# Kernel tuning notes

Measured on AMD Instinct MI355X. Metric: run time of the kernel, lower is better.

## Reference

```python
import jax, jax.numpy as jnp
import numpy as np

B, T, F, H = 256, 512, 8, 256
DEC_STEPS = 35
BN_EPS = 1e-3


def setup_inputs() -> dict:
    key = jax.random.key(0)
    ks = jax.random.split(key, 16)
    s = 0.05
    return {
        "pulse": jax.random.normal(ks[0], (B, T, F), jnp.float32),
        "bn_gamma": jax.random.uniform(ks[1], (F,), jnp.float32, 0.5, 1.5),
        "bn_beta": jax.random.normal(ks[2], (F,), jnp.float32) * s,
        "bn_mean": jax.random.normal(ks[3], (F,), jnp.float32) * s,
        "bn_var": jax.random.uniform(ks[4], (F,), jnp.float32, 0.5, 1.5),
        "W_pe": jax.random.normal(ks[5], (F, H), jnp.float32) * s,
        "b_pe": jax.random.normal(ks[6], (H,), jnp.float32) * s,
        "embed_table": jax.random.normal(ks[7], (1, H), jnp.float32) * s,
        "W_x": jax.random.normal(ks[8], (H, 4 * H), jnp.float32) * s,
        "W_h": jax.random.normal(ks[9], (H, 4 * H), jnp.float32) * s,
        "b_lstm": jax.random.normal(ks[10], (4 * H,), jnp.float32) * s,
        "W_mlp": jax.random.normal(ks[11], (H, 2), jnp.float32) * s,
        "b_mlp": jax.random.normal(ks[12], (2,), jnp.float32) * s,
        "scale_w": jax.random.normal(ks[13], (1, 1, 2), jnp.float32),
        "scale_b": jax.random.normal(ks[14], (1, 1, 2), jnp.float32),
    }


def _lstm_cell(x, h, c, W_x, W_h, b):
    # Keras LSTMCell: gate order i, f, g(cell), o
    z = x @ W_x + h @ W_h + b  # (B, 4H)
    i, f, g, o = jnp.split(z, 4, axis=-1)
    i, f, o = jax.nn.sigmoid(i), jax.nn.sigmoid(f), jax.nn.sigmoid(o)
    g = jnp.tanh(g)
    c_new = f * c + i * g
    h_new = o * jnp.tanh(c_new)
    return h_new, c_new


def reference(pulse, bn_gamma, bn_beta, bn_mean, bn_var, W_pe, b_pe,
              embed_table, W_x, W_h, b_lstm, W_mlp, b_mlp, scale_w, scale_b):
    b_, t_, _ = pulse.shape
    # BatchNorm (inference form, axis=-1, eps=1e-3)
    x = (pulse - bn_mean) * jax.lax.rsqrt(bn_var + BN_EPS) * bn_gamma + bn_beta
    pe = x @ W_pe + b_pe  # (B, T, H)

    def enc_step(carry, xt):
        h, c = carry
        h, c = _lstm_cell(xt, h, c, W_x, W_h, b_lstm)
        return (h, c), None

    h0 = jnp.zeros((b_, H), pulse.dtype)
    (h, c), _ = jax.lax.scan(enc_step, (h0, h0), pe.transpose(1, 0, 2))

    # sequence from the same encoder state each iteration; deterministically
    inp0 = jnp.broadcast_to(embed_table[0], (b_, H))

    def dec_step(carry, _):
        h, c, inp = carry
        h, c = _lstm_cell(inp, h, c, W_x, W_h, b_lstm)
        return (h, c, h), h

    _, hs = jax.lax.scan(dec_step, (h, c, inp0), None, length=DEC_STEPS)
    hs = hs.transpose(1, 0, 2)  # (B, 35, H) == eis_embed[:, 1:, :]

    pred = hs @ W_mlp + b_mlp  # (B, 35, 2) == pred[:, 1:, :]
    eis = pred * scale_w + scale_b
    return eis
```

## Files before the change

### kernel.cpp

```cpp
#include <hip/hip_runtime.h>
#include <hip/hip_bf16.h>
#include <hip/hip_fp16.h>
#include <stdint.h>

#define BB  256
#define TT  512
#define FF  8
#define HH  256
#define H4  1024
#define DEC 35
#define NWG 16
#define MW  16

typedef __attribute__((ext_vector_type(8))) short short8v;
typedef __attribute__((ext_vector_type(4))) float f32x4;

#define OFF_WPX  0
#define OFF_HHI  65536
#define OFF_HLO  81920
#define OFF_MLP  98304
#define OFF_SM   100352
#define OFF_HB32 100384
#define SMEM_TOT 116832

__device__ __forceinline__ unsigned short f2bf(float x) {
    unsigned u = __float_as_uint(x);
    u += 0x7fffu + ((u >> 16) & 1u);
    return (unsigned short)(u >> 16);
}
__device__ __forceinline__ float bf2f(unsigned s) { return __uint_as_float(s << 16); }
__device__ __forceinline__ float sigf(float x) {
    x = fminf(fmaxf(x, -30.f), 30.f);
    return 1.0f / (1.0f + __expf(-x));
}
__device__ __forceinline__ float tanh_(float x) {
    x = fminf(fmaxf(x, -15.f), 15.f);
    float e = __expf(2.0f * x);
    return (e - 1.0f) / (e + 1.0f);
}


__global__ void prep_consts(const float* __restrict__ W_pe, const float* __restrict__ b_pe,
                            const float* __restrict__ embed, const float* __restrict__ W_x,
                            const float* __restrict__ b_lstm,
                            const float* __restrict__ bn_gamma, const float* __restrict__ bn_beta,
                            const float* __restrict__ bn_mean, const float* __restrict__ bn_var,
                            float* __restrict__ Wpx32, float* __restrict__ zbias,
                            float* __restrict__ zdec0) {
    int n = blockIdx.x * 256 + threadIdx.x;
    float acc[FF];
    #pragma unroll
    for (int f = 0; f < FF; ++f) acc[f] = 0.f;
    float bsum = 0.f, dsum = 0.f;
    for (int m = 0; m < HH; ++m) {
        float wx = W_x[m * H4 + n];
        #pragma unroll
        for (int f = 0; f < FF; ++f) acc[f] = fmaf(W_pe[f * HH + m], wx, acc[f]);
        bsum = fmaf(b_pe[m], wx, bsum);
        dsum = fmaf(embed[m], wx, dsum);
    }
    float zb = b_lstm[n] + bsum;
    #pragma unroll
    for (int f = 0; f < FF; ++f) {
        float s  = bn_gamma[f] * rsqrtf(bn_var[f] + 1e-3f);
        float sh = bn_beta[f] - bn_mean[f] * s;
        Wpx32[f * H4 + n] = s * acc[f];
        zb = fmaf(sh, acc[f], zb);
    }
    zbias[n] = zb;
    zdec0[n] = b_lstm[n] + dsum;
}

__global__ void prep_wfrag(const float* __restrict__ W_x, const float* __restrict__ W_h,
                           short8v* __restrict__ whf, short8v* __restrict__ wsf) {
    int nt = blockIdx.x >> 3, kc = blockIdx.x & 7, ln = threadIdx.x;
    int n = nt * 16 + (ln & 15), q = ln >> 4;
    short8v vh, vs;
    #pragma unroll
    for (int j = 0; j < 8; ++j) {
        int k = kc * 32 + q * 8 + j;
        float wh = W_h[k * H4 + n], wx = W_x[k * H4 + n];
        vh[j] = (short)f2bf(wh);
        vs[j] = (short)f2bf(wx + wh);
    }
    whf[blockIdx.x * 64 + ln] = vh;
    wsf[blockIdx.x * 64 + ln] = vs;
}

__global__ void prep_wpxf(const float* __restrict__ Wpx32, short8v* __restrict__ wpxf) {
    int nt = blockIdx.x, ln = threadIdx.x;
    int n = nt * 16 + (ln & 15), qq = ln >> 4;
    short8v v;
    #pragma unroll
    for (int j = 0; j < 8; ++j) {
        float wv = Wpx32[j * H4 + n];
        unsigned short hi = f2bf(wv);
        v[j] = (qq < 2) ? (short)hi : (short)f2bf(wv - bf2f(hi));
    }
    wpxf[nt * 64 + ln] = v;
}

__global__ __launch_bounds__(512) void lstm_rec10(
    const short8v* __restrict__ whf, const short8v* __restrict__ wsf,
    const short8v* __restrict__ wpxf,
    const float* __restrict__ pulse,
    const float* __restrict__ zbias, const float* __restrict__ zdec0,
    const float* __restrict__ blstm,
    const float* __restrict__ W_mlp, const float* __restrict__ b_mlp,
    const float* __restrict__ scale_w, const float* __restrict__ scale_b,
    float* __restrict__ out) {
    extern __shared__ char smem[];
    short8v* ldsWPX = (short8v*)(smem + OFF_WPX);
    short8v* ldsHI  = (short8v*)(smem + OFF_HHI);
    short8v* ldsLO  = (short8v*)(smem + OFF_HLO);
    float*   sWmlp  = (float*)(smem + OFF_MLP);
    float*   sm     = (float*)(smem + OFF_SM);
    float*   hb32   = (float*)(smem + OFF_HB32);

    const int tid = threadIdx.x, g = blockIdx.x;
    const int w = tid >> 6, ln = tid & 63;
    const int col = ln & 15, q = ln >> 4;

    int ntv[8];
    #pragma unroll
    for (int tl = 0; tl < 8; ++tl) ntv[tl] = (tl >> 1) * 16 + 2 * w + (tl & 1);

    for (int i = tid; i < 64 * 64; i += 512) ldsWPX[i] = wpxf[i];
    {
        short8v zz = {};
        for (int i = tid; i < 2 * 512; i += 512) { ldsHI[i] = zz; ldsLO[i] = zz; }
    }
    for (int i = tid; i < HH * 2; i += 512) sWmlp[i] = W_mlp[i];
    if (tid < 2) { sm[tid] = b_mlp[tid]; sm[2 + tid] = scale_w[tid]; sm[4 + tid] = scale_b[tid]; }

    float zb[8];
    #pragma unroll
    for (int tl = 0; tl < 8; ++tl) zb[tl] = zbias[ntv[tl] * 16 + col];

    float c[8];
    #pragma unroll
    for (int i = 0; i < 8; ++i) c[i] = 0.f;

    const float* ppt = pulse + ((size_t)(g * MW + (ln & 15)) * TT) * FF;
    const int lohalf = q & 1;
    int rb = 0;
    __syncthreads();

#define CHAIN4(SRC, TL0) do {                                                   \
        short8v ws0[4], ws1[4];                                                 \
        _Pragma("unroll")                                                       \
        for (int i = 0; i < 4; ++i) {                                           \
            ws0[i] = (SRC)[(size_t)(ntv[(TL0) + i] * 8 + 0) * 64 + ln];         \
            ws1[i] = (SRC)[(size_t)(ntv[(TL0) + i] * 8 + 1) * 64 + ln];         \
        }                                                                       \
        _Pragma("unroll")                                                       \
        for (int kc = 0; kc < 8; ++kc) {                                        \
            short8v ah = ldsHI[rb * 512 + kc * 64 + ln];                        \
            short8v al = ldsLO[rb * 512 + kc * 64 + ln];                        \
            if ((kc & 1) == 0) {                                                \
                _Pragma("unroll")                                               \
                for (int i = 0; i < 4; ++i) {                                   \
                    acc[(TL0) + i] = __builtin_amdgcn_mfma_f32_16x16x32_bf16(ah, ws0[i], acc[(TL0) + i], 0, 0, 0); \
                    acc[(TL0) + i] = __builtin_amdgcn_mfma_f32_16x16x32_bf16(al, ws0[i], acc[(TL0) + i], 0, 0, 0); \
                    if (kc + 2 < 8) ws0[i] = (SRC)[(size_t)(ntv[(TL0) + i] * 8 + kc + 2) * 64 + ln]; \
                }                                                               \
            } else {                                                            \
                _Pragma("unroll")                                               \
                for (int i = 0; i < 4; ++i) {                                   \
                    acc[(TL0) + i] = __builtin_amdgcn_mfma_f32_16x16x32_bf16(ah, ws1[i], acc[(TL0) + i], 0, 0, 0); \
                    acc[(TL0) + i] = __builtin_amdgcn_mfma_f32_16x16x32_bf16(al, ws1[i], acc[(TL0) + i], 0, 0, 0); \
                    if (kc + 2 < 8) ws1[i] = (SRC)[(size_t)(ntv[(TL0) + i] * 8 + kc + 2) * 64 + ln]; \
                }                                                               \
            }                                                                   \
        }                                                                       \
    } while (0)

#define GATES_WRITE(WITH_HB32) do {                                             \
        unsigned short* hHIs = (unsigned short*)(smem + OFF_HHI) + (rb ^ 1) * 4096; \
        unsigned short* hLOs = (unsigned short*)(smem + OFF_HLO) + (rb ^ 1) * 4096; \
        _Pragma("unroll")                                                       \
        for (int p = 0; p < 2; ++p)                                             \
            _Pragma("unroll")                                                   \
            for (int r = 0; r < 4; ++r) {                                       \
                float cc = sigf(acc[2 + p][r]) * c[p * 4 + r] + sigf(acc[p][r]) * tanh_(acc[4 + p][r]); \
                c[p * 4 + r] = cc;                                              \
                float hh = sigf(acc[6 + p][r]) * tanh_(cc);                     \
                unsigned short hi = f2bf(hh);                                   \
                float lo = hh - bf2f(hi);                                       \
                int ad = w * 512 + (2 * p + (col >> 3)) * 128 + (4 * q + r) * 8 + (col & 7); \
                hHIs[ad] = hi;                                                  \
                hLOs[ad] = f2bf(lo);                                            \
                if (WITH_HB32) hb32[(4 * q + r) * 257 + (32 * w + 16 * p + col)] = hh; \
            }                                                                   \
    } while (0)

    for (int t = 0; t < TT; ++t) {
        float4 p0 = ((const float4*)ppt)[0];
        float4 p1 = ((const float4*)ppt)[1];
        ppt += FF;
        float pv[8];
        pv[0] = p0.x; pv[1] = p0.y; pv[2] = p0.z; pv[3] = p0.w;
        pv[4] = p1.x; pv[5] = p1.y; pv[6] = p1.z; pv[7] = p1.w;
        short8v apack;
        #pragma unroll
        for (int j = 0; j < 8; ++j) {
            unsigned short hi = f2bf(pv[j]);
            apack[j] = lohalf ? (short)f2bf(pv[j] - bf2f(hi)) : (short)hi;
        }

        f32x4 acc[8];
        #pragma unroll
        for (int tl = 0; tl < 8; ++tl) {
            f32x4 av; av[0] = zb[tl]; av[1] = zb[tl]; av[2] = zb[tl]; av[3] = zb[tl];
            short8v bw = ldsWPX[ntv[tl] * 64 + ln];
            acc[tl] = __builtin_amdgcn_mfma_f32_16x16x32_bf16(apack, bw, av, 0, 0, 0);
        }
        CHAIN4(whf, 0);
        CHAIN4(whf, 4);
        GATES_WRITE(0);
        __syncthreads();
        rb ^= 1;
    }

    float zd0[8], bl[8];
    #pragma unroll
    for (int tl = 0; tl < 8; ++tl) {
        zd0[tl] = zdec0[ntv[tl] * 16 + col];
        bl[tl]  = blstm[ntv[tl] * 16 + col];
    }

    for (int s = 0; s < DEC; ++s) {
        f32x4 acc[8];
        if (s == 0) {
            #pragma unroll
            for (int tl = 0; tl < 8; ++tl) {
                f32x4 av; av[0] = zd0[tl]; av[1] = zd0[tl]; av[2] = zd0[tl]; av[3] = zd0[tl];
                acc[tl] = av;
            }
            CHAIN4(whf, 0);
            CHAIN4(whf, 4);
        } else {
            #pragma unroll
            for (int tl = 0; tl < 8; ++tl) {
                f32x4 av; av[0] = bl[tl]; av[1] = bl[tl]; av[2] = bl[tl]; av[3] = bl[tl];
                acc[tl] = av;
            }
            CHAIN4(wsf, 0);
            CHAIN4(wsf, 4);
        }
        GATES_WRITE(1);
        __syncthreads();

        {
            int m = tid >> 5, j = (tid >> 4) & 1, uc = tid & 15;
            float p2 = 0.f;
            #pragma unroll
            for (int i = 0; i < 16; ++i) {
                int u = i * 16 + uc;
                p2 = fmaf(hb32[m * 257 + u], sWmlp[u * 2 + j], p2);
            }
            p2 += __shfl_down(p2, 8, 16);
            p2 += __shfl_down(p2, 4, 16);
            p2 += __shfl_down(p2, 2, 16);
            p2 += __shfl_down(p2, 1, 16);
            if (uc == 0) {
                float pr = p2 + sm[j];
                out[((size_t)(g * MW + m) * DEC + s) * 2 + j] = pr * sm[2 + j] + sm[4 + j];
            }
        }
        __syncthreads();
        rb ^= 1;
    }
#undef CHAIN4
#undef GATES_WRITE
}

__global__ void prep_weights(const float* __restrict__ Wx, const float* __restrict__ Wh,
                             __hip_bfloat16* __restrict__ wxb,
                             __hip_bfloat16* __restrict__ whb,
                             __hip_bfloat16* __restrict__ wsb) {
    int i = blockIdx.x * 256 + threadIdx.x;
    if (i < HH * H4) {
        float x = Wx[i], h = Wh[i];
        wxb[i] = __float2bfloat16(x);
        whb[i] = __float2bfloat16(h);
        wsb[i] = __float2bfloat16(x + h);
    }
}

template<bool BF16W>
__device__ __forceinline__ void matvec2(const void* __restrict__ W,
                                        const float* __restrict__ vec,
                                        int tid, float& z0, float& z1) {
    if constexpr (BF16W) {
        const uint32_t* Wp = (const uint32_t*)W;
        #pragma unroll 8
        for (int k = 0; k < HH; ++k) {
            uint32_t w = Wp[(size_t)k * (H4 / 2) + tid];
            float s = vec[k];
            union { uint32_t u; float f; } lo, hi;
            lo.u = w << 16;
            hi.u = w & 0xffff0000u;
            z0 = fmaf(s, lo.f, z0);
            z1 = fmaf(s, hi.f, z1);
        }
    } else {
        const float2* Wp = (const float2*)W;
        #pragma unroll 8
        for (int k = 0; k < HH; ++k) {
            float2 w = Wp[(size_t)k * (H4 / 2) + tid];
            float s = vec[k];
            z0 = fmaf(s, w.x, z0);
            z1 = fmaf(s, w.y, z1);
        }
    }
}

__device__ __forceinline__ float sigmoidf_(float x) { return 1.0f / (1.0f + expf(-x)); }

template<bool BF16W>
__global__ __launch_bounds__(512)
void lstm_persist(const float* __restrict__ pulse,
                  const float* __restrict__ bn_gamma, const float* __restrict__ bn_beta,
                  const float* __restrict__ bn_mean, const float* __restrict__ bn_var,
                  const float* __restrict__ W_pe, const float* __restrict__ b_pe,
                  const float* __restrict__ embed,
                  const float* __restrict__ W_x, const float* __restrict__ W_h,
                  const float* __restrict__ b_lstm,
                  const float* __restrict__ W_mlp, const float* __restrict__ b_mlp,
                  const float* __restrict__ scale_w, const float* __restrict__ scale_b,
                  const void* __restrict__ WxQ, const void* __restrict__ WhQ,
                  const void* __restrict__ WsQ,
                  float* __restrict__ out) {
    __shared__ float sWpe2[FF * HH];
    __shared__ float sbpe2[HH];
    __shared__ float sbl[H4];
    __shared__ float sWmlp[HH * 2];
    __shared__ float sbuf[HH];
    __shared__ float hbuf[HH];
    __shared__ float cbuf[HH];
    __shared__ float zbuf[H4];
    __shared__ float bnsc[FF], bnsh[FF];
    __shared__ float smisc[6];

    const int tid = threadIdx.x;
    const int bb  = blockIdx.x;

    if (tid < FF) {
        float s = bn_gamma[tid] * rsqrtf(bn_var[tid] + 1e-3f);
        bnsc[tid] = s;
        bnsh[tid] = bn_beta[tid] - bn_mean[tid] * s;
    }
    if (tid < 2) {
        smisc[tid]     = b_mlp[tid];
        smisc[2 + tid] = scale_w[tid];
        smisc[4 + tid] = scale_b[tid];
    }
    for (int i = tid; i < H4; i += 512) sbl[i] = b_lstm[i];
    for (int i = tid; i < 2 * HH; i += 512) sWmlp[i] = W_mlp[i];
    for (int i = tid; i < HH; i += 512) { hbuf[i] = 0.f; cbuf[i] = 0.f; }
    __syncthreads();
    for (int i = tid; i < FF * HH; i += 512) sWpe2[i] = W_pe[i] * bnsc[i / HH];
    for (int i = tid; i < HH; i += 512) {
        float a = b_pe[i];
        #pragma unroll
        for (int f = 0; f < FF; ++f) a = fmaf(bnsh[f], W_pe[f * HH + i], a);
        sbpe2[i] = a;
    }
    __syncthreads();
    if (tid >= HH && tid < 2 * HH) {
        int u = tid - HH;
        const float* pr = pulse + (size_t)bb * TT * FF;
        float acc = sbpe2[u];
        #pragma unroll
        for (int f = 0; f < FF; ++f) acc = fmaf(pr[f], sWpe2[f * HH + u], acc);
        sbuf[u] = acc;
    }
    __syncthreads();

    for (int t = 0; t < TT; ++t) {
        float z0 = sbl[2 * tid], z1 = sbl[2 * tid + 1];
        if constexpr (BF16W) {
            matvec2<true>(WxQ, sbuf, tid, z0, z1);
            matvec2<true>(WhQ, hbuf, tid, z0, z1);
        } else {
            matvec2<false>(W_x, sbuf, tid, z0, z1);
            matvec2<false>(W_h, hbuf, tid, z0, z1);
        }
        zbuf[2 * tid] = z0; zbuf[2 * tid + 1] = z1;
        __syncthreads();
        if (tid < HH) {
            float iv = zbuf[tid], fv = zbuf[tid + HH];
            float gv = zbuf[tid + 2 * HH], ov = zbuf[tid + 3 * HH];
            float c = sigmoidf_(fv) * cbuf[tid] + sigmoidf_(iv) * tanhf(gv);
            cbuf[tid] = c;
            hbuf[tid] = sigmoidf_(ov) * tanhf(c);
        } else if (tid < 2 * HH) {
            int u = tid - HH;
            float acc;
            if (t + 1 < TT) {
                const float* pr = pulse + ((size_t)bb * TT + (t + 1)) * FF;
                acc = sbpe2[u];
                #pragma unroll
                for (int f = 0; f < FF; ++f) acc = fmaf(pr[f], sWpe2[f * HH + u], acc);
            } else {
                acc = embed[u];
            }
            sbuf[u] = acc;
        }
        __syncthreads();
    }

    for (int s = 0; s < DEC; ++s) {
        float z0 = sbl[2 * tid], z1 = sbl[2 * tid + 1];
        if (s == 0) {
            if constexpr (BF16W) {
                matvec2<true>(WxQ, sbuf, tid, z0, z1);
                matvec2<true>(WhQ, hbuf, tid, z0, z1);
            } else {
                matvec2<false>(W_x, sbuf, tid, z0, z1);
                matvec2<false>(W_h, hbuf, tid, z0, z1);
            }
        } else {
            if constexpr (BF16W) {
                matvec2<true>(WsQ, hbuf, tid, z0, z1);
            } else {
                matvec2<false>(W_x, hbuf, tid, z0, z1);
                matvec2<false>(W_h, hbuf, tid, z0, z1);
            }
        }
        zbuf[2 * tid] = z0; zbuf[2 * tid + 1] = z1;
        __syncthreads();
        if (tid < HH) {
            float iv = zbuf[tid], fv = zbuf[tid + HH];
            float gv = zbuf[tid + 2 * HH], ov = zbuf[tid + 3 * HH];
            float c = sigmoidf_(fv) * cbuf[tid] + sigmoidf_(iv) * tanhf(gv);
            cbuf[tid] = c;
            hbuf[tid] = sigmoidf_(ov) * tanhf(c);
        }
        __syncthreads();
        if (tid < 128) {
            int j = tid >> 6, lane = tid & 63;
            float p = 0.f;
            #pragma unroll
            for (int u = lane; u < HH; u += 64) p = fmaf(hbuf[u], sWmlp[u * 2 + j], p);
            p += __shfl_down(p, 32); p += __shfl_down(p, 16); p += __shfl_down(p, 8);
            p += __shfl_down(p, 4);  p += __shfl_down(p, 2);  p += __shfl_down(p, 1);
            if (lane == 0) {
                float pr2 = p + smisc[j];
                out[((size_t)bb * DEC + s) * 2 + j] = pr2 * smisc[2 + j] + smisc[4 + j];
            }
        }
        __syncthreads();
    }
}

extern "C" void kernel_launch(void* const* d_in, const int* in_sizes, int n_in,
                              void* d_out, int out_size, void* d_ws, size_t ws_size,
                              hipStream_t stream) {
    const float* pulse    = (const float*)d_in[0];
    const float* bn_gamma = (const float*)d_in[1];
    const float* bn_beta  = (const float*)d_in[2];
    const float* bn_mean  = (const float*)d_in[3];
    const float* bn_var   = (const float*)d_in[4];
    const float* W_pe     = (const float*)d_in[5];
    const float* b_pe     = (const float*)d_in[6];
    const float* embed    = (const float*)d_in[7];
    const float* W_x      = (const float*)d_in[8];
    const float* W_h      = (const float*)d_in[9];
    const float* b_lstm   = (const float*)d_in[10];
    const float* W_mlp    = (const float*)d_in[11];
    const float* b_mlp    = (const float*)d_in[12];
    const float* scale_w  = (const float*)d_in[13];
    const float* scale_b  = (const float*)d_in[14];
    float* out = (float*)d_out;

    const size_t SZ_WF   = (size_t)64 * 8 * 64 * 16;
    const size_t SZ_PXF  = (size_t)64 * 64 * 16;
    const size_t SZ_PX32 = (size_t)FF * H4 * 4;
    const size_t needA = 2 * SZ_WF + SZ_PXF + SZ_PX32 + 2 * (size_t)H4 * 4;

    if (ws_size >= needA) {
        short8v* whf   = (short8v*)d_ws;
        short8v* wsf   = (short8v*)((char*)d_ws + SZ_WF);
        short8v* wpxf  = (short8v*)((char*)d_ws + 2 * SZ_WF);
        float*   Wpx32 = (float*)((char*)d_ws + 2 * SZ_WF + SZ_PXF);
        float*   zbias = Wpx32 + FF * H4;
        float*   zdec0 = zbias + H4;

        hipFuncSetAttribute((const void*)lstm_rec10,
                            hipFuncAttributeMaxDynamicSharedMemorySize, SMEM_TOT);

        prep_consts<<<4, 256, 0, stream>>>(W_pe, b_pe, embed, W_x, b_lstm,
                                           bn_gamma, bn_beta, bn_mean, bn_var,
                                           Wpx32, zbias, zdec0);
        prep_wfrag<<<512, 64, 0, stream>>>(W_x, W_h, whf, wsf);
        prep_wpxf<<<64, 64, 0, stream>>>(Wpx32, wpxf);
        lstm_rec10<<<NWG, 512, SMEM_TOT, stream>>>(whf, wsf, wpxf, pulse,
                                                   zbias, zdec0, b_lstm,
                                                   W_mlp, b_mlp, scale_w, scale_b, out);
        return;
    }

    const size_t NW = (size_t)HH * H4;
    bool use_bf16 = ws_size >= 3 * NW * sizeof(__hip_bfloat16);
    __hip_bfloat16* wxb = (__hip_bfloat16*)d_ws;
    __hip_bfloat16* whb = wxb + NW;
    __hip_bfloat16* wsb = whb + NW;

    if (use_bf16) {
        prep_weights<<<(int)((NW + 255) / 256), 256, 0, stream>>>(W_x, W_h, wxb, whb, wsb);
        lstm_persist<true><<<BB, 512, 0, stream>>>(
            pulse, bn_gamma, bn_beta, bn_mean, bn_var, W_pe, b_pe, embed,
            W_x, W_h, b_lstm, W_mlp, b_mlp, scale_w, scale_b,
            (const void*)wxb, (const void*)whb, (const void*)wsb, out);
    } else {
        lstm_persist<false><<<BB, 512, 0, stream>>>(
            pulse, bn_gamma, bn_beta, bn_mean, bn_var, W_pe, b_pe, embed,
            W_x, W_h, b_lstm, W_mlp, b_mlp, scale_w, scale_b,
            nullptr, nullptr, nullptr, out);
    }
}
```

Baseline: 5.401 ms.

## Split each batch group's LSTM across four workgroups with global-memory h exchange

The recurrent kernel used to run 16 workgroups of 512 threads, each holding all 1024 gate columns for 16 batch rows. It now launches 64 workgroups of 256 threads, with four workgroups sharing each batch group and each owning a quarter of the gate columns. Every step writes its h slice to global memory, then synchronises through an atomic counter spin barrier before reloading the full h into LDS. This spreads the weight streaming over four times as many CUs, at the cost of a cross-workgroup barrier and a global round trip on each of the 547 steps, and it relies on all 64 workgroups being resident at once.

```diff
diff --git a/kernel.cpp b/kernel.cpp
--- a/kernel.cpp
+++ b/kernel.cpp
@@ -9,19 +9,10 @@
 #define HH  256
 #define H4  1024
 #define DEC 35
-#define NWG 16
 #define MW  16
 
 typedef __attribute__((ext_vector_type(8))) short short8v;
 typedef __attribute__((ext_vector_type(4))) float f32x4;
-
-#define OFF_WPX  0
-#define OFF_HHI  65536
-#define OFF_HLO  81920
-#define OFF_MLP  98304
-#define OFF_SM   100352
-#define OFF_HB32 100384
-#define SMEM_TOT 116832
 
 __device__ __forceinline__ unsigned short f2bf(float x) {
     unsigned u = __float_as_uint(x);
@@ -100,7 +91,7 @@
     wpxf[nt * 64 + ln] = v;
 }
 
-__global__ __launch_bounds__(512) void lstm_rec10(
+__global__ __launch_bounds__(256) void lstm_rec12(
     const short8v* __restrict__ whf, const short8v* __restrict__ wsf,
     const short8v* __restrict__ wpxf,
     const float* __restrict__ pulse,
@@ -108,90 +99,113 @@
     const float* __restrict__ blstm,
     const float* __restrict__ W_mlp, const float* __restrict__ b_mlp,
     const float* __restrict__ scale_w, const float* __restrict__ scale_b,
+    unsigned short* __restrict__ hx, int* __restrict__ ctr,
     float* __restrict__ out) {
-    extern __shared__ char smem[];
-    short8v* ldsWPX = (short8v*)(smem + OFF_WPX);
-    short8v* ldsHI  = (short8v*)(smem + OFF_HHI);
-    short8v* ldsLO  = (short8v*)(smem + OFF_HLO);
-    float*   sWmlp  = (float*)(smem + OFF_MLP);
-    float*   sm     = (float*)(smem + OFF_SM);
-    float*   hb32   = (float*)(smem + OFF_HB32);
-
-    const int tid = threadIdx.x, g = blockIdx.x;
+    __shared__ short8v ldsHI[512];
+    __shared__ short8v ldsLO[512];
+    __shared__ float sWmlp[HH * 2];
+    __shared__ float sm[6];
+
+    const int tid = threadIdx.x, bx = blockIdx.x;
+    const int gb = bx >> 2, jj = bx & 3;
     const int w = tid >> 6, ln = tid & 63;
     const int col = ln & 15, q = ln >> 4;
-
-    int ntv[8];
-    #pragma unroll
-    for (int tl = 0; tl < 8; ++tl) ntv[tl] = (tl >> 1) * 16 + 2 * w + (tl & 1);
-
-    for (int i = tid; i < 64 * 64; i += 512) ldsWPX[i] = wpxf[i];
+    const int ut = jj * 4 + w;
+
+    int ntv[4];
+    #pragma unroll
+    for (int gg = 0; gg < 4; ++gg) ntv[gg] = gg * 16 + ut;
+
+    unsigned short* hxg = hx + (size_t)gb * 8192;
+
+    sWmlp[tid] = W_mlp[tid];
+    sWmlp[256 + tid] = W_mlp[256 + tid];
+    if (tid < 2) { sm[tid] = b_mlp[tid]; sm[2 + tid] = scale_w[tid]; sm[4 + tid] = scale_b[tid]; }
     {
         short8v zz = {};
-        for (int i = tid; i < 2 * 512; i += 512) { ldsHI[i] = zz; ldsLO[i] = zz; }
-    }
-    for (int i = tid; i < HH * 2; i += 512) sWmlp[i] = W_mlp[i];
-    if (tid < 2) { sm[tid] = b_mlp[tid]; sm[2 + tid] = scale_w[tid]; sm[4 + tid] = scale_b[tid]; }
-
-    float zb[8];
-    #pragma unroll
-    for (int tl = 0; tl < 8; ++tl) zb[tl] = zbias[ntv[tl] * 16 + col];
-
-    float c[8];
-    #pragma unroll
-    for (int i = 0; i < 8; ++i) c[i] = 0.f;
-
-    const float* ppt = pulse + ((size_t)(g * MW + (ln & 15)) * TT) * FF;
+        ldsHI[tid] = zz; ldsHI[256 + tid] = zz;
+        ldsLO[tid] = zz; ldsLO[256 + tid] = zz;
+    }
+    short8v wpxr[4];
+    float zb[4], zd0[4], bl[4];
+    #pragma unroll
+    for (int gg = 0; gg < 4; ++gg) {
+        wpxr[gg] = wpxf[(size_t)ntv[gg] * 64 + ln];
+        int n = ntv[gg] * 16 + col;
+        zb[gg]  = zbias[n];
+        zd0[gg] = zdec0[n];
+        bl[gg]  = blstm[n];
+    }
+    float c[4];
+    #pragma unroll
+    for (int i = 0; i < 4; ++i) c[i] = 0.f;
+
+    const float* ppt = pulse + ((size_t)(gb * MW + col) * TT) * FF;
     const int lohalf = q & 1;
-    int rb = 0;
+    int sync_no = 0;
     __syncthreads();
 
-#define CHAIN4(SRC, TL0) do {                                                   \
+#define CHAIN4(SRC) do {                                                        \
         short8v ws0[4], ws1[4];                                                 \
         _Pragma("unroll")                                                       \
         for (int i = 0; i < 4; ++i) {                                           \
-            ws0[i] = (SRC)[(size_t)(ntv[(TL0) + i] * 8 + 0) * 64 + ln];         \
-            ws1[i] = (SRC)[(size_t)(ntv[(TL0) + i] * 8 + 1) * 64 + ln];         \
+            ws0[i] = (SRC)[(size_t)(ntv[i] * 8 + 0) * 64 + ln];                 \
+            ws1[i] = (SRC)[(size_t)(ntv[i] * 8 + 1) * 64 + ln];                 \
         }                                                                       \
         _Pragma("unroll")                                                       \
         for (int kc = 0; kc < 8; ++kc) {                                        \
-            short8v ah = ldsHI[rb * 512 + kc * 64 + ln];                        \
-            short8v al = ldsLO[rb * 512 + kc * 64 + ln];                        \
+            short8v ah = ldsHI[kc * 64 + ln];                                   \
+            short8v al = ldsLO[kc * 64 + ln];                                   \
             if ((kc & 1) == 0) {                                                \
                 _Pragma("unroll")                                               \
                 for (int i = 0; i < 4; ++i) {                                   \
-                    acc[(TL0) + i] = __builtin_amdgcn_mfma_f32_16x16x32_bf16(ah, ws0[i], acc[(TL0) + i], 0, 0, 0); \
-                    acc[(TL0) + i] = __builtin_amdgcn_mfma_f32_16x16x32_bf16(al, ws0[i], acc[(TL0) + i], 0, 0, 0); \
-                    if (kc + 2 < 8) ws0[i] = (SRC)[(size_t)(ntv[(TL0) + i] * 8 + kc + 2) * 64 + ln]; \
+                    acc[i] = __builtin_amdgcn_mfma_f32_16x16x32_bf16(ah, ws0[i], acc[i], 0, 0, 0); \
+                    acc[i] = __builtin_amdgcn_mfma_f32_16x16x32_bf16(al, ws0[i], acc[i], 0, 0, 0); \
+                    if (kc + 2 < 8) ws0[i] = (SRC)[(size_t)(ntv[i] * 8 + kc + 2) * 64 + ln]; \
                 }                                                               \
             } else {                                                            \
                 _Pragma("unroll")                                               \
                 for (int i = 0; i < 4; ++i) {                                   \
-                    acc[(TL0) + i] = __builtin_amdgcn_mfma_f32_16x16x32_bf16(ah, ws1[i], acc[(TL0) + i], 0, 0, 0); \
-                    acc[(TL0) + i] = __builtin_amdgcn_mfma_f32_16x16x32_bf16(al, ws1[i], acc[(TL0) + i], 0, 0, 0); \
-                    if (kc + 2 < 8) ws1[i] = (SRC)[(size_t)(ntv[(TL0) + i] * 8 + kc + 2) * 64 + ln]; \
+                    acc[i] = __builtin_amdgcn_mfma_f32_16x16x32_bf16(ah, ws1[i], acc[i], 0, 0, 0); \
+                    acc[i] = __builtin_amdgcn_mfma_f32_16x16x32_bf16(al, ws1[i], acc[i], 0, 0, 0); \
+                    if (kc + 2 < 8) ws1[i] = (SRC)[(size_t)(ntv[i] * 8 + kc + 2) * 64 + ln]; \
                 }                                                               \
             }                                                                   \
         }                                                                       \
     } while (0)
 
-#define GATES_WRITE(WITH_HB32) do {                                             \
-        unsigned short* hHIs = (unsigned short*)(smem + OFF_HHI) + (rb ^ 1) * 4096; \
-        unsigned short* hLOs = (unsigned short*)(smem + OFF_HLO) + (rb ^ 1) * 4096; \
+#define GATES_STORE() do {                                                      \
         _Pragma("unroll")                                                       \
-        for (int p = 0; p < 2; ++p)                                             \
-            _Pragma("unroll")                                                   \
-            for (int r = 0; r < 4; ++r) {                                       \
-                float cc = sigf(acc[2 + p][r]) * c[p * 4 + r] + sigf(acc[p][r]) * tanh_(acc[4 + p][r]); \
-                c[p * 4 + r] = cc;                                              \
-                float hh = sigf(acc[6 + p][r]) * tanh_(cc);                     \
-                unsigned short hi = f2bf(hh);                                   \
-                float lo = hh - bf2f(hi);                                       \
-                int ad = w * 512 + (2 * p + (col >> 3)) * 128 + (4 * q + r) * 8 + (col & 7); \
-                hHIs[ad] = hi;                                                  \
-                hLOs[ad] = f2bf(lo);                                            \
-                if (WITH_HB32) hb32[(4 * q + r) * 257 + (32 * w + 16 * p + col)] = hh; \
-            }                                                                   \
+        for (int r = 0; r < 4; ++r) {                                           \
+            float cc = sigf(acc[1][r]) * c[r] + sigf(acc[0][r]) * tanh_(acc[2][r]); \
+            c[r] = cc;                                                          \
+            float hh = sigf(acc[3][r]) * tanh_(cc);                             \
+            unsigned short hi = f2bf(hh);                                       \
+            float lo = hh - bf2f(hi);                                           \
+            int u = ut * 16 + col, b = 4 * q + r;                               \
+            int ad = (u >> 5) * 512 + ((u >> 3) & 3) * 128 + b * 8 + (u & 7);   \
+            hxg[ad] = hi;                                                       \
+            hxg[4096 + ad] = f2bf(lo);                                          \
+        }                                                                       \
+    } while (0)
+
+#define EXCHANGE() do {                                                         \
+        __threadfence();                                                        \
+        __syncthreads();                                                        \
+        ++sync_no;                                                              \
+        if (tid == 0) {                                                         \
+            atomicAdd(ctr + gb, 1);                                             \
+            while (atomicAdd(ctr + gb, 0) < 4 * sync_no)                        \
+                __builtin_amdgcn_s_sleep(1);                                    \
+        }                                                                       \
+        __syncthreads();                                                        \
+        __threadfence();                                                        \
+        const short8v* hxv = (const short8v*)hxg;                               \
+        ldsHI[tid]       = hxv[tid];                                            \
+        ldsHI[256 + tid] = hxv[256 + tid];                                      \
+        ldsLO[tid]       = hxv[512 + tid];                                      \
+        ldsLO[256 + tid] = hxv[768 + tid];                                      \
+        __syncthreads();                                                        \
     } while (0)
 
     for (int t = 0; t < TT; ++t) {
@@ -207,72 +221,61 @@
             unsigned short hi = f2bf(pv[j]);
             apack[j] = lohalf ? (short)f2bf(pv[j] - bf2f(hi)) : (short)hi;
         }
-
-        f32x4 acc[8];
+        f32x4 acc[4];
         #pragma unroll
-        for (int tl = 0; tl < 8; ++tl) {
-            f32x4 av; av[0] = zb[tl]; av[1] = zb[tl]; av[2] = zb[tl]; av[3] = zb[tl];
-            short8v bw = ldsWPX[ntv[tl] * 64 + ln];
-            acc[tl] = __builtin_amdgcn_mfma_f32_16x16x32_bf16(apack, bw, av, 0, 0, 0);
-        }
-        CHAIN4(whf, 0);
-        CHAIN4(whf, 4);
-        GATES_WRITE(0);
-        __syncthreads();
-        rb ^= 1;
-    }
-
-    float zd0[8], bl[8];
-    #pragma unroll
-    for (int tl = 0; tl < 8; ++tl) {
-        zd0[tl] = zdec0[ntv[tl] * 16 + col];
-        bl[tl]  = blstm[ntv[tl] * 16 + col];
+        for (int gg = 0; gg < 4; ++gg) {
+            f32x4 av; av[0] = zb[gg]; av[1] = zb[gg]; av[2] = zb[gg]; av[3] = zb[gg];
+            acc[gg] = __builtin_amdgcn_mfma_f32_16x16x32_bf16(apack, wpxr[gg], av, 0, 0, 0);
+        }
+        CHAIN4(whf);
+        GATES_STORE();
+        EXCHANGE();
     }
 
     for (int s = 0; s < DEC; ++s) {
-        f32x4 acc[8];
+        f32x4 acc[4];
         if (s == 0) {
             #pragma unroll
-            for (int tl = 0; tl < 8; ++tl) {
-                f32x4 av; av[0] = zd0[tl]; av[1] = zd0[tl]; av[2] = zd0[tl]; av[3] = zd0[tl];
-                acc[tl] = av;
-            }
-            CHAIN4(whf, 0);
-            CHAIN4(whf, 4);
+            for (int gg = 0; gg < 4; ++gg) {
+                f32x4 av; av[0] = zd0[gg]; av[1] = zd0[gg]; av[2] = zd0[gg]; av[3] = zd0[gg];
+                acc[gg] = av;
+            }
+            CHAIN4(whf);
         } else {
             #pragma unroll
-            for (int tl = 0; tl < 8; ++tl) {
-                f32x4 av; av[0] = bl[tl]; av[1] = bl[tl]; av[2] = bl[tl]; av[3] = bl[tl];
-                acc[tl] = av;
-            }
-            CHAIN4(wsf, 0);
-            CHAIN4(wsf, 4);
-        }
-        GATES_WRITE(1);
-        __syncthreads();
-
-        {
-            int m = tid >> 5, j = (tid >> 4) & 1, uc = tid & 15;
+            for (int gg = 0; gg < 4; ++gg) {
+                f32x4 av; av[0] = bl[gg]; av[1] = bl[gg]; av[2] = bl[gg]; av[3] = bl[gg];
+                acc[gg] = av;
+            }
+            CHAIN4(wsf);
+        }
+        GATES_STORE();
+        EXCHANGE();
+
+        if (jj == 0) {
+            const unsigned short* hHIs = (const unsigned short*)ldsHI;
+            const unsigned short* hLOs = (const unsigned short*)ldsLO;
+            int m = tid >> 4, j2 = (tid >> 3) & 1, uc = tid & 7;
             float p2 = 0.f;
             #pragma unroll
-            for (int i = 0; i < 16; ++i) {
-                int u = i * 16 + uc;
-                p2 = fmaf(hb32[m * 257 + u], sWmlp[u * 2 + j], p2);
-            }
-            p2 += __shfl_down(p2, 8, 16);
-            p2 += __shfl_down(p2, 4, 16);
-            p2 += __shfl_down(p2, 2, 16);
-            p2 += __shfl_down(p2, 1, 16);
+            for (int i = 0; i < 32; ++i) {
+                int u = i * 8 + uc;
+                int ad = (u >> 5) * 512 + ((u >> 3) & 3) * 128 + m * 8 + (u & 7);
+                float hv = bf2f(hHIs[ad]) + bf2f(hLOs[ad]);
+                p2 = fmaf(hv, sWmlp[u * 2 + j2], p2);
+            }
+            p2 += __shfl_down(p2, 4, 8);
+            p2 += __shfl_down(p2, 2, 8);
+            p2 += __shfl_down(p2, 1, 8);
             if (uc == 0) {
-                float pr = p2 + sm[j];
-                out[((size_t)(g * MW + m) * DEC + s) * 2 + j] = pr * sm[2 + j] + sm[4 + j];
-            }
-        }
-        __syncthreads();
-        rb ^= 1;
+                float pr = p2 + sm[j2];
+                out[((size_t)(gb * MW + m) * DEC + s) * 2 + j2] = pr * sm[2 + j2] + sm[4 + j2];
+            }
+        }
     }
 #undef CHAIN4
-#undef GATES_WRITE
+#undef GATES_STORE
+#undef EXCHANGE
 }
 
 __global__ void prep_weights(const float* __restrict__ Wx, const float* __restrict__ Wh,
@@ -476,29 +479,35 @@
     float* out = (float*)d_out;
 
     const size_t SZ_WF   = (size_t)64 * 8 * 64 * 16;
-    const size_t SZ_PXF  = (size_t)64 * 64 * 16;
-    const size_t SZ_PX32 = (size_t)FF * H4 * 4;
-    const size_t needA = 2 * SZ_WF + SZ_PXF + SZ_PX32 + 2 * (size_t)H4 * 4;
+    const size_t OFF_WSF = SZ_WF;
+    const size_t OFF_PXF = 2 * SZ_WF;
+    const size_t OFF_P32 = OFF_PXF + 65536;
+    const size_t OFF_ZB  = OFF_P32 + 32768;
+    const size_t OFF_ZD  = OFF_ZB + 4096;
+    const size_t OFF_HX  = OFF_ZD + 4096;
+    const size_t OFF_CTR = OFF_HX + 262144;
+    const size_t needA   = OFF_CTR + 256;
 
     if (ws_size >= needA) {
         short8v* whf   = (short8v*)d_ws;
-        short8v* wsf   = (short8v*)((char*)d_ws + SZ_WF);
-        short8v* wpxf  = (short8v*)((char*)d_ws + 2 * SZ_WF);
-        float*   Wpx32 = (float*)((char*)d_ws + 2 * SZ_WF + SZ_PXF);
-        float*   zbias = Wpx32 + FF * H4;
-        float*   zdec0 = zbias + H4;
-
-        hipFuncSetAttribute((const void*)lstm_rec10,
-                            hipFuncAttributeMaxDynamicSharedMemorySize, SMEM_TOT);
-
+        short8v* wsf   = (short8v*)((char*)d_ws + OFF_WSF);
+        short8v* wpxf  = (short8v*)((char*)d_ws + OFF_PXF);
+        float*   Wpx32 = (float*)((char*)d_ws + OFF_P32);
+        float*   zbias = (float*)((char*)d_ws + OFF_ZB);
+        float*   zdec0 = (float*)((char*)d_ws + OFF_ZD);
+        unsigned short* hx = (unsigned short*)((char*)d_ws + OFF_HX);
+        int*     ctr   = (int*)((char*)d_ws + OFF_CTR);
+
+        hipMemsetAsync(ctr, 0, 256, stream);
         prep_consts<<<4, 256, 0, stream>>>(W_pe, b_pe, embed, W_x, b_lstm,
                                            bn_gamma, bn_beta, bn_mean, bn_var,
                                            Wpx32, zbias, zdec0);
         prep_wfrag<<<512, 64, 0, stream>>>(W_x, W_h, whf, wsf);
         prep_wpxf<<<64, 64, 0, stream>>>(Wpx32, wpxf);
-        lstm_rec10<<<NWG, 512, SMEM_TOT, stream>>>(whf, wsf, wpxf, pulse,
-                                                   zbias, zdec0, b_lstm,
-                                                   W_mlp, b_mlp, scale_w, scale_b, out);
+        lstm_rec12<<<64, 256, 0, stream>>>(whf, wsf, wpxf, pulse,
+                                           zbias, zdec0, b_lstm,
+                                           W_mlp, b_mlp, scale_w, scale_b,
+                                           hx, ctr, out);
         return;
     }
 
```

After: 7.411 ms. +37.2%, slower.
